# Performance work log

Measured on AMD Instinct MI355X. Metric: run time of the kernel, lower is better.

The kernel has to match this reference:

```python
import jax, jax.numpy as jnp
import numpy as np
from jax import lax

# Model dims (match init_kwargs)
D, K, V, H, R = 256, 16, 64, 4, 23
B, HH, WW = 16, 64, 64
EPS = 1e-5


def setup_inputs() -> dict:
    key = jax.random.key(0)
    ks = jax.random.split(key, 6)
    s = 0.05
    x = jax.random.normal(ks[0], (B, D, HH, WW), dtype=jnp.float32)
    Wq = jax.random.normal(ks[1], (H * K, D), dtype=jnp.float32) * s
    Wk = jax.random.normal(ks[2], (K, D), dtype=jnp.float32) * s
    Wv = jax.random.normal(ks[3], (V, D), dtype=jnp.float32) * s
    conv_w = jax.random.normal(ks[4], (K, 1, R, 1), dtype=jnp.float32) * s  # Conv2d(1, k, (r,1))
    conv_b = jnp.zeros((K,), jnp.float32)
    # BatchNorm (inference-mode) params for query and value branches
    q_gamma = jnp.ones((H * K,), jnp.float32)
    q_beta = jnp.zeros((H * K,), jnp.float32)
    q_mean = jnp.zeros((H * K,), jnp.float32)
    q_var = jnp.ones((H * K,), jnp.float32)
    v_gamma = jnp.ones((V,), jnp.float32)
    v_beta = jnp.zeros((V,), jnp.float32)
    v_mean = jnp.zeros((V,), jnp.float32)
    v_var = jnp.ones((V,), jnp.float32)
    return dict(x=x, Wq=Wq, q_gamma=q_gamma, q_beta=q_beta, q_mean=q_mean, q_var=q_var,
                Wk=Wk, Wv=Wv, v_gamma=v_gamma, v_beta=v_beta, v_mean=v_mean, v_var=v_var,
                conv_w=conv_w, conv_b=conv_b)


def _bn(y, g, b_, m, v_):
    # y: (b, c, n); per-channel affine normalization (eval-mode BatchNorm)
    scale = (g * lax.rsqrt(v_ + EPS))[None, :, None]
    return (y - m[None, :, None]) * scale + b_[None, :, None]


def reference(x, Wq, q_gamma, q_beta, q_mean, q_var, Wk, Wv, v_gamma, v_beta, v_mean, v_var, conv_w, conv_b):
    b, d, h, w = x.shape
    n = h * w
    xf = x.reshape(b, d, n)  # (b, d, n)

    # query: 1x1 conv -> BN -> (b, H, n, K)
    q = _bn(jnp.einsum('od,bdn->bon', Wq, xf), q_gamma, q_beta, q_mean, q_var)
    q = q.reshape(b, H, K, n).transpose(0, 1, 3, 2)  # (b, H, n, K)

    # key: 1x1 conv -> softmax over positions -> (b, n, K)
    kk = jax.nn.softmax(jnp.einsum('od,bdn->bon', Wk, xf), axis=-1).transpose(0, 2, 1)

    # value: 1x1 conv -> BN -> (b, n, V)
    vv = _bn(jnp.einsum('od,bdn->bon', Wv, xf), v_gamma, v_beta, v_mean, v_var).transpose(0, 2, 1)

    # content lambda: (b, K, V)
    lam_c = jnp.einsum('bmk,bmv->bkv', kk, vv)

    # position lambda via local conv over positions: (b, n, K, V)
    pad = (R - 1) // 2
    lam_p = lax.conv_general_dilated(
        vv[:, None, :, :], conv_w, window_strides=(1, 1),
        padding=[(pad, pad), (0, 0)],
        dimension_numbers=('NCHW', 'OIHW', 'NCHW'))  # (b, K, n, V)
    lam_p = lam_p + conv_b[None, :, None, None]
    lam_p = lam_p.transpose(0, 2, 1, 3)  # (b, n, K, V)

    # apply lambdas per position: (b, n, H, V)
    out = jnp.einsum('bhnk,bnkv->bnhv', q, lam_c[:, None, :, :] + lam_p)
    return out.reshape(b, h, w, H * V).transpose(0, 3, 1, 2)  # (b, H*V, h, w)
```

## Files before the change

### kernel.cpp

```cpp
#include <hip/hip_runtime.h>
#include <hip/hip_bf16.h>

typedef unsigned int uint;
typedef unsigned short ushort;

#define Bn 16
#define Dd 256
#define Nn 4096
#define Hh 4
#define Kk 16
#define Vv 64
#define Rr 23
#define Cc 144
#define NRT 9

typedef short bf16x8s __attribute__((ext_vector_type(8)));
typedef float f32x4 __attribute__((ext_vector_type(4)));
typedef float f32x8 __attribute__((ext_vector_type(8)));

static __device__ __forceinline__ ushort f2bf(float f) {
    __hip_bfloat16 h = __float2bfloat16(f);
    return __builtin_bit_cast(ushort, h);
}
static __device__ __forceinline__ float bf2f(ushort u) {
    return __uint_as_float(((uint)u) << 16);
}
static __device__ __forceinline__ float bflo(uint u) { return __uint_as_float(u << 16); }
static __device__ __forceinline__ float bfhi(uint u) { return __uint_as_float(u & 0xffff0000u); }

__global__ __launch_bounds__(256) void pack_kernel(
    const float* __restrict__ Wq, const float* __restrict__ qg, const float* __restrict__ qb,
    const float* __restrict__ qm, const float* __restrict__ qv,
    const float* __restrict__ Wk, const float* __restrict__ Wv,
    const float* __restrict__ vg, const float* __restrict__ vb,
    const float* __restrict__ vm, const float* __restrict__ vvar,
    const float* __restrict__ conv_w,
    ushort* __restrict__ Wf16, float* __restrict__ bias,
    ushort* __restrict__ cwf, float* __restrict__ num, float* __restrict__ den) {
    int c = blockIdx.x;
    int t = threadIdx.x;
    int d = t;
    float scale, bs;
    const float* src;
    if (c < 64) {
        scale = qg[c] * rsqrtf(qv[c] + 1e-5f);
        bs = qb[c] - qm[c] * scale;
        src = Wq + c * Dd;
    } else if (c < 80) {
        scale = 1.f; bs = 0.f;
        src = Wk + (c - 64) * Dd;
    } else {
        int j = c - 80;
        scale = vg[j] * rsqrtf(vvar[j] + 1e-5f);
        bs = vb[j] - vm[j] * scale;
        src = Wv + j * Dd;
    }
    int rt = c >> 4, lm = c & 15;
    int kk = d >> 5, hi = (d >> 3) & 3, j = d & 7;
    Wf16[((rt * 8 + kk) * 64 + hi * 16 + lm) * 8 + j] = f2bf(src[d] * scale);
    if (d == 0) bias[c] = bs;

    if (c == 0) {
#pragma unroll
        for (int m = 0; m < 4; m++) {
            int flat = t + 256 * m;
            int mt = flat >> 9, rem = flat & 511;
            int l = rem >> 3, jj = rem & 7;
            int r = mt * 16 + (l & 15);
            int k = (l >> 4) * 8 + jj;
            float v = (r < Rr && k < Kk) ? conv_w[k * Rr + r] : 0.f;
            cwf[flat] = f2bf(v);
        }
    }
    if (c == 1) {
        float4 z = {0.f, 0.f, 0.f, 0.f};
#pragma unroll
        for (int m = 0; m < 16; m++)
            reinterpret_cast<float4*>(num)[t + 256 * m] = z;
        if (t < 64) reinterpret_cast<float4*>(den)[t] = z;
    }
}

__global__ __launch_bounds__(256, 4) void proj_mfma_kernel(
    const float* __restrict__ x, const ushort* __restrict__ Wf16,
    const float* __restrict__ bias,
    ushort* __restrict__ qbufT, ushort* __restrict__ vbufT,
    float* __restrict__ num, float* __restrict__ den) {
    __shared__ ushort Wlds[NRT * 2 * 64 * 8];

    int b = blockIdx.y;
    int n0 = blockIdx.x * 64;
    int t = threadIdx.x;
    int w = t >> 6, l = t & 63;
    int lm = l & 15, hi = l >> 4;
    int n = n0 + w * 16 + lm;

    const uint* WfU = (const uint*)Wf16;
    uint* WldsU = (uint*)Wlds;

    f32x4 acc[NRT];
#pragma unroll
    for (int rt = 0; rt < NRT; rt++) acc[rt] = (f32x4){0.f, 0.f, 0.f, 0.f};

    const float* xb = x + (size_t)b * Dd * Nn + n;

    auto load8 = [&](int kk) -> f32x8 {
        const float* xp = xb + (size_t)(kk * 32 + hi * 8) * Nn;
        f32x8 r;
        r[0] = xp[0];
        r[1] = xp[(size_t)1 * Nn];
        r[2] = xp[(size_t)2 * Nn];
        r[3] = xp[(size_t)3 * Nn];
        r[4] = xp[(size_t)4 * Nn];
        r[5] = xp[(size_t)5 * Nn];
        r[6] = xp[(size_t)6 * Nn];
        r[7] = xp[(size_t)7 * Nn];
        return r;
    };
    auto cvt8 = [&](f32x8 f) -> bf16x8s {
        bf16x8s o;
#pragma unroll
        for (int j = 0; j < 8; j++) o[j] = (short)f2bf(f[j]);
        return o;
    };

    f32x8 xc0 = load8(0), xc1 = load8(1);
    f32x8 xn0 = xc0, xn1 = xc1;

#pragma unroll
    for (int p = 0; p < 4; p++) {
        int kb = p * 2;
        if (p) __syncthreads();
#pragma unroll
        for (int i = 0; i < 18; i++) {
            int flat = t + 256 * i;
            int f2 = flat >> 8;
            int rt = f2 >> 1, kkl = f2 & 1;
            WldsU[flat] = WfU[((rt * 8 + kb + kkl) << 8) + (flat & 255)];
        }
        __syncthreads();

        bf16x8s bf0 = cvt8(xc0);
        bf16x8s bf1 = cvt8(xc1);
        if (p < 3) {
            xn0 = load8(kb + 2);
            xn1 = load8(kb + 3);
        }
#pragma unroll
        for (int rt = 0; rt < NRT; rt++) {
            bf16x8s afrag = *reinterpret_cast<const bf16x8s*>(
                &Wlds[(size_t)((rt * 2 + 0) * 64 + l) * 8]);
            acc[rt] = __builtin_amdgcn_mfma_f32_16x16x32_bf16(afrag, bf0, acc[rt], 0, 0, 0);
        }
#pragma unroll
        for (int rt = 0; rt < NRT; rt++) {
            bf16x8s afrag = *reinterpret_cast<const bf16x8s*>(
                &Wlds[(size_t)((rt * 2 + 1) * 64 + l) * 8]);
            acc[rt] = __builtin_amdgcn_mfma_f32_16x16x32_bf16(afrag, bf1, acc[rt], 0, 0, 0);
        }
        xc0 = xn0;
        xc1 = xn1;
    }

    __syncthreads();
    {
        int nl = w * 16 + lm;
#pragma unroll
        for (int rt = 0; rt < 4; rt++)
#pragma unroll
            for (int rr = 0; rr < 4; rr++) {
                int kq = hi * 4 + rr;
                Wlds[nl * 72 + kq * 4 + rt] = f2bf(acc[rt][rr] + bias[rt * 16 + kq]);
            }
#pragma unroll
        for (int rt = 5; rt < 9; rt++)
#pragma unroll
            for (int rr = 0; rr < 4; rr++) {
                int v = (rt - 5) * 16 + hi * 4 + rr;
                Wlds[4608 + nl * 72 + v] = f2bf(acc[rt][rr] + bias[80 + v]);
            }
    }
    __syncthreads();

#pragma unroll
    for (int m = 0; m < 2; m++) {
        int i = t + 256 * m;
        int row = i >> 3, seg = i & 7;
        uint4 u = *reinterpret_cast<const uint4*>(&Wlds[row * 72 + seg * 8]);
        *reinterpret_cast<uint4*>(&qbufT[((size_t)b * Nn + n0 + row) * 64 + seg * 8]) = u;
    }
#pragma unroll
    for (int m = 0; m < 2; m++) {
        int i = t + 256 * m;
        int row = i >> 3, seg = i & 7;
        uint4 u = *reinterpret_cast<const uint4*>(&Wlds[4608 + row * 72 + seg * 8]);
        *reinterpret_cast<uint4*>(&vbufT[((size_t)b * Nn + n0 + row) * 64 + seg * 8]) = u;
    }

    float ev[4];
#pragma unroll
    for (int rr = 0; rr < 4; rr++)
        ev[rr] = __expf(acc[4][rr] + bias[64 + hi * 4 + rr]);
    __syncthreads();
    float* eks = reinterpret_cast<float*>(Wlds);
    {
        int nl = w * 16 + lm;
#pragma unroll
        for (int rr = 0; rr < 4; rr++)
            eks[(hi * 4 + rr) * 64 + nl] = ev[rr];
    }
    __syncthreads();
    {
        int v = t & 63, k0 = t >> 6;
        float a4[4] = {0.f, 0.f, 0.f, 0.f};
        for (int nl = 0; nl < 64; nl++) {
            float wv = bf2f(Wlds[4608 + nl * 72 + v]);
#pragma unroll
            for (int j2 = 0; j2 < 4; j2++)
                a4[j2] += eks[(k0 + 4 * j2) * 64 + nl] * wv;
        }
#pragma unroll
        for (int j2 = 0; j2 < 4; j2++)
            atomicAdd(&num[((size_t)b * Kk + k0 + 4 * j2) * Vv + v], a4[j2]);
        if (t < Kk) {
            float s = 0.f;
#pragma unroll
            for (int nl = 0; nl < 64; nl++) s += eks[t * 64 + nl];
            atomicAdd(&den[(size_t)b * Kk + t], s);
        }
    }
}

#define TN 32
__global__ __launch_bounds__(256, 4) void fused_out_kernel(
    const ushort* __restrict__ qbufT, const ushort* __restrict__ vbufT,
    const ushort* __restrict__ cwf, const float* __restrict__ num,
    const float* __restrict__ den, const float* __restrict__ conv_b,
    float* __restrict__ out) {
    __shared__ ushort Af[12 * 64 * 8];
    __shared__ ushort Sf[4][12 * 32 * 8];
    __shared__ ushort Qf[4][2 * 64 * 8];

    int b = blockIdx.y;
    int n0 = blockIdx.x * TN;
    int t = threadIdx.x;
    int l = t & 63;

    uint4 vld0 = {0, 0, 0, 0}, vld1 = {0, 0, 0, 0};
    {
        int c = t >> 3, vg = t & 7;
        int n = n0 - 11 + c;
        if (n >= 0 && n < Nn)
            vld0 = *reinterpret_cast<const uint4*>(&vbufT[((size_t)b * Nn + n) * 64 + vg * 8]);
        int i2 = t + 256;
        if (i2 < 432) {
            int c2 = i2 >> 3, vg2 = i2 & 7;
            int n2 = n0 - 11 + c2;
            if (n2 >= 0 && n2 < Nn)
                vld1 = *reinterpret_cast<const uint4*>(&vbufT[((size_t)b * Nn + n2) * 64 + vg2 * 8]);
        }
    }
    uint2 qld0, qld1;
    {
        int i = t;
        qld0 = *reinterpret_cast<const uint2*>(
            &qbufT[((size_t)b * Nn + n0 + (i & 31)) * 64 + (i >> 5) * 4]);
        int i2 = t + 256;
        qld1 = *reinterpret_cast<const uint2*>(
            &qbufT[((size_t)b * Nn + n0 + (i2 & 31)) * 64 + (i2 >> 5) * 4]);
    }
    uint4 cwld0 = *reinterpret_cast<const uint4*>(&cwf[(0 * 64 + l) * 8]);
    uint4 cwld1 = *reinterpret_cast<const uint4*>(&cwf[(1 * 64 + l) * 8]);
    float4 lcl = *reinterpret_cast<const float4*>(&num[(size_t)b * Kk * Vv + t * 4]);
    float dk = den[(size_t)b * Kk + (t >> 4)];
    float cb = conv_b[t >> 4];

    uint4 z4 = {0, 0, 0, 0};
    reinterpret_cast<uint4*>(Af)[512 + t] = z4;
#pragma unroll
    for (int m = 0; m < 6; m++) reinterpret_cast<uint4*>(Sf)[t + 256 * m] = z4;
#pragma unroll
    for (int m = 0; m < 2; m++) reinterpret_cast<uint4*>(Qf)[t + 256 * m] = z4;
    __syncthreads();

    {
        int c = t >> 3, vg = t & 7;
        int kk = c >> 5, hi = (c >> 3) & 3, j = c & 7;
        ushort* base = &Af[((kk * 4 + hi) * 64 + vg * 8) * 8 + j];
        uint va[4] = {vld0.x, vld0.y, vld0.z, vld0.w};
#pragma unroll
        for (int e = 0; e < 4; e++) {
            base[(2 * e + 0) * 8] = (ushort)(va[e] & 0xffff);
            base[(2 * e + 1) * 8] = (ushort)(va[e] >> 16);
        }
        int i2 = t + 256;
        if (i2 < 432) {
            int c2 = i2 >> 3, vg2 = i2 & 7;
            int kk2 = c2 >> 5, hi2 = (c2 >> 3) & 3, j2 = c2 & 7;
            ushort* base2 = &Af[((kk2 * 4 + hi2) * 64 + vg2 * 8) * 8 + j2];
            uint vb4[4] = {vld1.x, vld1.y, vld1.z, vld1.w};
#pragma unroll
            for (int e = 0; e < 4; e++) {
                base2[(2 * e + 0) * 8] = (ushort)(vb4[e] & 0xffff);
                base2[(2 * e + 1) * 8] = (ushort)(vb4[e] >> 16);
            }
        }
    }
    {
        int k = t >> 4, v0 = (t & 15) * 4;
        int c = 54 + k;
        int kk = c >> 5, hi = (c >> 3) & 3, j = c & 7;
        ushort* base = &Af[((kk * 4 + hi) * 64 + v0) * 8 + j];
        float inv = 1.f / dk;
        base[0]  = f2bf(lcl.x * inv + cb);
        base[8]  = f2bf(lcl.y * inv + cb);
        base[16] = f2bf(lcl.z * inv + cb);
        base[24] = f2bf(lcl.w * inv + cb);
    }
    {
        int i = t;
        {
            int k = i >> 5, nl = i & 31, m = 54 + k;
            int kk = m >> 5, hi = (m >> 3) & 3, j = m & 7;
            int off = ((kk * 4 + hi) * 32 + nl) * 8 + j;
            Sf[0][off] = (ushort)(qld0.x & 0xffff);
            Sf[1][off] = (ushort)(qld0.x >> 16);
            Sf[2][off] = (ushort)(qld0.y & 0xffff);
            Sf[3][off] = (ushort)(qld0.y >> 16);
            int nt = nl >> 4, lmq = nl & 15;
            int qoff = (nt * 64 + (k >> 3) * 16 + lmq) * 8 + (k & 7);
            Qf[0][qoff] = (ushort)(qld0.x & 0xffff);
            Qf[1][qoff] = (ushort)(qld0.x >> 16);
            Qf[2][qoff] = (ushort)(qld0.y & 0xffff);
            Qf[3][qoff] = (ushort)(qld0.y >> 16);
        }
        int i2 = t + 256;
        {
            int k = i2 >> 5, nl = i2 & 31, m = 54 + k;
            int kk = m >> 5, hi = (m >> 3) & 3, j = m & 7;
            int off = ((kk * 4 + hi) * 32 + nl) * 8 + j;
            Sf[0][off] = (ushort)(qld1.x & 0xffff);
            Sf[1][off] = (ushort)(qld1.x >> 16);
            Sf[2][off] = (ushort)(qld1.y & 0xffff);
            Sf[3][off] = (ushort)(qld1.y >> 16);
            int nt = nl >> 4, lmq = nl & 15;
            int qoff = (nt * 64 + (k >> 3) * 16 + lmq) * 8 + (k & 7);
            Qf[0][qoff] = (ushort)(qld1.x & 0xffff);
            Qf[1][qoff] = (ushort)(qld1.x >> 16);
            Qf[2][qoff] = (ushort)(qld1.y & 0xffff);
            Qf[3][qoff] = (ushort)(qld1.y >> 16);
        }
    }
    __syncthreads();

    int h = t >> 6;
    int lm = l & 15, hif = l >> 4;
    {
        bf16x8s cwfr0 = __builtin_bit_cast(bf16x8s, cwld0);
        bf16x8s cwfr1 = __builtin_bit_cast(bf16x8s, cwld1);
        f32x4 gacc[2][2];
#pragma unroll
        for (int nt = 0; nt < 2; nt++) {
            bf16x8s qfr = *reinterpret_cast<const bf16x8s*>(&Qf[h][(nt * 64 + l) * 8]);
            gacc[0][nt] = __builtin_amdgcn_mfma_f32_16x16x32_bf16(
                cwfr0, qfr, (f32x4){0.f, 0.f, 0.f, 0.f}, 0, 0, 0);
            gacc[1][nt] = __builtin_amdgcn_mfma_f32_16x16x32_bf16(
                cwfr1, qfr, (f32x4){0.f, 0.f, 0.f, 0.f}, 0, 0, 0);
        }
#pragma unroll
        for (int mt = 0; mt < 2; mt++)
#pragma unroll
            for (int nt = 0; nt < 2; nt++)
#pragma unroll
                for (int rr = 0; rr < 4; rr++) {
                    int r = mt * 16 + hif * 4 + rr;
                    if (r < Rr) {
                        int nl2 = nt * 16 + lm;
                        int m = nl2 + r;
                        Sf[h][((m >> 3) * 32 + nl2) * 8 + (m & 7)] = f2bf(gacc[mt][nt][rr]);
                    }
                }
    }
    __syncthreads();

    f32x4 acc[4][2];
#pragma unroll
    for (int mt = 0; mt < 4; mt++)
#pragma unroll
        for (int nt = 0; nt < 2; nt++) acc[mt][nt] = (f32x4){0.f, 0.f, 0.f, 0.f};

#pragma unroll
    for (int kk = 0; kk < 3; kk++) {
        bf16x8s bfr[2];
#pragma unroll
        for (int nt = 0; nt < 2; nt++)
            bfr[nt] = *reinterpret_cast<const bf16x8s*>(
                &Sf[h][((kk * 4 + hif) * 32 + nt * 16 + lm) * 8]);
#pragma unroll
        for (int mt = 0; mt < 4; mt++) {
            bf16x8s afr = *reinterpret_cast<const bf16x8s*>(
                &Af[((kk * 4 + hif) * 64 + mt * 16 + lm) * 8]);
#pragma unroll
            for (int nt = 0; nt < 2; nt++)
                acc[mt][nt] = __builtin_amdgcn_mfma_f32_16x16x32_bf16(afr, bfr[nt], acc[mt][nt], 0, 0, 0);
        }
    }

    float* ob = out + ((size_t)b * 256 + h * 64) * Nn + n0;
#pragma unroll
    for (int mt = 0; mt < 4; mt++)
#pragma unroll
        for (int nt = 0; nt < 2; nt++)
#pragma unroll
            for (int rr = 0; rr < 4; rr++) {
                int v = mt * 16 + hif * 4 + rr;
                ob[(size_t)v * Nn + nt * 16 + lm] = acc[mt][nt][rr];
            }
}

extern "C" void kernel_launch(void* const* d_in, const int* in_sizes, int n_in,
                              void* d_out, int out_size, void* d_ws, size_t ws_size,
                              hipStream_t stream) {
    const float* x      = (const float*)d_in[0];
    const float* Wq     = (const float*)d_in[1];
    const float* qg     = (const float*)d_in[2];
    const float* qb     = (const float*)d_in[3];
    const float* qm     = (const float*)d_in[4];
    const float* qv     = (const float*)d_in[5];
    const float* Wk     = (const float*)d_in[6];
    const float* Wv     = (const float*)d_in[7];
    const float* vg     = (const float*)d_in[8];
    const float* vb     = (const float*)d_in[9];
    const float* vm     = (const float*)d_in[10];
    const float* vvar   = (const float*)d_in[11];
    const float* conv_w = (const float*)d_in[12];
    const float* conv_b = (const float*)d_in[13];
    float* out = (float*)d_out;

    float* wsf = (float*)d_ws;
    ushort* Wf16  = (ushort*)wsf;
    float*  bias  = wsf + 18432;
    float*  num   = wsf + 18688;
    float*  den   = wsf + 35072;
    ushort* cwf   = (ushort*)(wsf + 35328);
    ushort* qbufT = (ushort*)(wsf + 35840);
    ushort* vbufT = (ushort*)(wsf + 2132992);

    pack_kernel<<<Cc, 256, 0, stream>>>(Wq, qg, qb, qm, qv, Wk, Wv, vg, vb, vm, vvar,
                                        conv_w, Wf16, bias, cwf, num, den);
    proj_mfma_kernel<<<dim3(Nn / 64, Bn), 256, 0, stream>>>(x, Wf16, bias,
                                                            qbufT, vbufT, num, den);
    fused_out_kernel<<<dim3(Nn / TN, Bn), 256, 0, stream>>>(qbufT, vbufT, cwf, num, den,
                                                            conv_b, out);
}
```

Measured before the change: 47.33 us.

## Shrink fused output kernel position tile from 32 to 16

Halves the number of positions each block of the fused output kernel handles. The shared-memory layout is rebuilt for the smaller tile: the halo window plus the lambda rows now fit in a reduction depth of 64 instead of 96, so two MFMA k-steps replace three. The aim is less wasted padding in the reduction and more blocks for latency hiding. The cost is twice as many blocks, a larger relative halo overhead on the value loads, and 16-wide output stores that coalesce less well.

```diff
diff --git a/kernel.cpp b/kernel.cpp
--- a/kernel.cpp
+++ b/kernel.cpp
@@ -231,15 +231,15 @@
     }
 }
 
-#define TN 32
+#define TN 16
 __global__ __launch_bounds__(256, 4) void fused_out_kernel(
     const ushort* __restrict__ qbufT, const ushort* __restrict__ vbufT,
     const ushort* __restrict__ cwf, const float* __restrict__ num,
     const float* __restrict__ den, const float* __restrict__ conv_b,
     float* __restrict__ out) {
-    __shared__ ushort Af[12 * 64 * 8];
-    __shared__ ushort Sf[4][12 * 32 * 8];
-    __shared__ ushort Qf[4][2 * 64 * 8];
+    __shared__ ushort Af[8 * 64 * 8];
+    __shared__ ushort Sf[4][8 * 16 * 8];
+    __shared__ ushort Qf[4][64 * 8];
 
     int b = blockIdx.y;
     int n0 = blockIdx.x * TN;
@@ -248,26 +248,23 @@
 
     uint4 vld0 = {0, 0, 0, 0}, vld1 = {0, 0, 0, 0};
     {
-        int c = t >> 3, vg = t & 7;
-        int n = n0 - 11 + c;
+        int j = t >> 3, seg = t & 7;
+        int n = n0 - 11 + j;
         if (n >= 0 && n < Nn)
-            vld0 = *reinterpret_cast<const uint4*>(&vbufT[((size_t)b * Nn + n) * 64 + vg * 8]);
+            vld0 = *reinterpret_cast<const uint4*>(&vbufT[((size_t)b * Nn + n) * 64 + seg * 8]);
         int i2 = t + 256;
-        if (i2 < 432) {
-            int c2 = i2 >> 3, vg2 = i2 & 7;
-            int n2 = n0 - 11 + c2;
+        if (i2 < 304) {
+            int j2 = i2 >> 3, seg2 = i2 & 7;
+            int n2 = n0 - 11 + j2;
             if (n2 >= 0 && n2 < Nn)
-                vld1 = *reinterpret_cast<const uint4*>(&vbufT[((size_t)b * Nn + n2) * 64 + vg2 * 8]);
-        }
-    }
-    uint2 qld0, qld1;
-    {
-        int i = t;
-        qld0 = *reinterpret_cast<const uint2*>(
-            &qbufT[((size_t)b * Nn + n0 + (i & 31)) * 64 + (i >> 5) * 4]);
-        int i2 = t + 256;
-        qld1 = *reinterpret_cast<const uint2*>(
-            &qbufT[((size_t)b * Nn + n0 + (i2 & 31)) * 64 + (i2 >> 5) * 4]);
+                vld1 = *reinterpret_cast<const uint4*>(&vbufT[((size_t)b * Nn + n2) * 64 + seg2 * 8]);
+        }
+    }
+    uint2 qld;
+    {
+        int nl = t >> 4, k = t & 15;
+        qld = *reinterpret_cast<const uint2*>(
+            &qbufT[((size_t)b * Nn + n0 + nl) * 64 + k * 4]);
     }
     uint4 cwld0 = *reinterpret_cast<const uint4*>(&cwf[(0 * 64 + l) * 8]);
     uint4 cwld1 = *reinterpret_cast<const uint4*>(&cwf[(1 * 64 + l) * 8]);
@@ -276,17 +273,16 @@
     float cb = conv_b[t >> 4];
 
     uint4 z4 = {0, 0, 0, 0};
-    reinterpret_cast<uint4*>(Af)[512 + t] = z4;
-#pragma unroll
-    for (int m = 0; m < 6; m++) reinterpret_cast<uint4*>(Sf)[t + 256 * m] = z4;
-#pragma unroll
-    for (int m = 0; m < 2; m++) reinterpret_cast<uint4*>(Qf)[t + 256 * m] = z4;
-    __syncthreads();
-
-    {
-        int c = t >> 3, vg = t & 7;
-        int kk = c >> 5, hi = (c >> 3) & 3, j = c & 7;
-        ushort* base = &Af[((kk * 4 + hi) * 64 + vg * 8) * 8 + j];
+    reinterpret_cast<uint4*>(Af)[t]       = z4;
+    reinterpret_cast<uint4*>(Af)[t + 256] = z4;
+    reinterpret_cast<uint4*>(Sf)[t]       = z4;
+    reinterpret_cast<uint4*>(Sf)[t + 256] = z4;
+    reinterpret_cast<uint4*>(Qf)[t]       = z4;
+    __syncthreads();
+
+    {
+        int c = t >> 3, seg = t & 7;
+        ushort* base = &Af[((c >> 3) * 64 + seg * 8) * 8 + (c & 7)];
         uint va[4] = {vld0.x, vld0.y, vld0.z, vld0.w};
 #pragma unroll
         for (int e = 0; e < 4; e++) {
@@ -294,10 +290,9 @@
             base[(2 * e + 1) * 8] = (ushort)(va[e] >> 16);
         }
         int i2 = t + 256;
-        if (i2 < 432) {
-            int c2 = i2 >> 3, vg2 = i2 & 7;
-            int kk2 = c2 >> 5, hi2 = (c2 >> 3) & 3, j2 = c2 & 7;
-            ushort* base2 = &Af[((kk2 * 4 + hi2) * 64 + vg2 * 8) * 8 + j2];
+        if (i2 < 304) {
+            int c2 = i2 >> 3, seg2 = i2 & 7;
+            ushort* base2 = &Af[((c2 >> 3) * 64 + seg2 * 8) * 8 + (c2 & 7)];
             uint vb4[4] = {vld1.x, vld1.y, vld1.z, vld1.w};
 #pragma unroll
             for (int e = 0; e < 4; e++) {
@@ -308,9 +303,8 @@
     }
     {
         int k = t >> 4, v0 = (t & 15) * 4;
-        int c = 54 + k;
-        int kk = c >> 5, hi = (c >> 3) & 3, j = c & 7;
-        ushort* base = &Af[((kk * 4 + hi) * 64 + v0) * 8 + j];
+        int c = 38 + k;
+        ushort* base = &Af[((c >> 3) * 64 + v0) * 8 + (c & 7)];
         float inv = 1.f / dk;
         base[0]  = f2bf(lcl.x * inv + cb);
         base[8]  = f2bf(lcl.y * inv + cb);
@@ -318,38 +312,18 @@
         base[24] = f2bf(lcl.w * inv + cb);
     }
     {
-        int i = t;
-        {
-            int k = i >> 5, nl = i & 31, m = 54 + k;
-            int kk = m >> 5, hi = (m >> 3) & 3, j = m & 7;
-            int off = ((kk * 4 + hi) * 32 + nl) * 8 + j;
-            Sf[0][off] = (ushort)(qld0.x & 0xffff);
-            Sf[1][off] = (ushort)(qld0.x >> 16);
-            Sf[2][off] = (ushort)(qld0.y & 0xffff);
-            Sf[3][off] = (ushort)(qld0.y >> 16);
-            int nt = nl >> 4, lmq = nl & 15;
-            int qoff = (nt * 64 + (k >> 3) * 16 + lmq) * 8 + (k & 7);
-            Qf[0][qoff] = (ushort)(qld0.x & 0xffff);
-            Qf[1][qoff] = (ushort)(qld0.x >> 16);
-            Qf[2][qoff] = (ushort)(qld0.y & 0xffff);
-            Qf[3][qoff] = (ushort)(qld0.y >> 16);
-        }
-        int i2 = t + 256;
-        {
-            int k = i2 >> 5, nl = i2 & 31, m = 54 + k;
-            int kk = m >> 5, hi = (m >> 3) & 3, j = m & 7;
-            int off = ((kk * 4 + hi) * 32 + nl) * 8 + j;
-            Sf[0][off] = (ushort)(qld1.x & 0xffff);
-            Sf[1][off] = (ushort)(qld1.x >> 16);
-            Sf[2][off] = (ushort)(qld1.y & 0xffff);
-            Sf[3][off] = (ushort)(qld1.y >> 16);
-            int nt = nl >> 4, lmq = nl & 15;
-            int qoff = (nt * 64 + (k >> 3) * 16 + lmq) * 8 + (k & 7);
-            Qf[0][qoff] = (ushort)(qld1.x & 0xffff);
-            Qf[1][qoff] = (ushort)(qld1.x >> 16);
-            Qf[2][qoff] = (ushort)(qld1.y & 0xffff);
-            Qf[3][qoff] = (ushort)(qld1.y >> 16);
-        }
+        int nl = t >> 4, k = t & 15;
+        int m = 38 + k;
+        int off = ((m >> 3) * 16 + nl) * 8 + (m & 7);
+        Sf[0][off] = (ushort)(qld.x & 0xffff);
+        Sf[1][off] = (ushort)(qld.x >> 16);
+        Sf[2][off] = (ushort)(qld.y & 0xffff);
+        Sf[3][off] = (ushort)(qld.y >> 16);
+        int qoff = ((k >> 3) * 16 + nl) * 8 + (k & 7);
+        Qf[0][qoff] = (ushort)(qld.x & 0xffff);
+        Qf[1][qoff] = (ushort)(qld.x >> 16);
+        Qf[2][qoff] = (ushort)(qld.y & 0xffff);
+        Qf[3][qoff] = (ushort)(qld.y >> 16);
     }
     __syncthreads();
 
@@ -358,51 +332,41 @@
     {
         bf16x8s cwfr0 = __builtin_bit_cast(bf16x8s, cwld0);
         bf16x8s cwfr1 = __builtin_bit_cast(bf16x8s, cwld1);
-        f32x4 gacc[2][2];
-#pragma unroll
-        for (int nt = 0; nt < 2; nt++) {
-            bf16x8s qfr = *reinterpret_cast<const bf16x8s*>(&Qf[h][(nt * 64 + l) * 8]);
-            gacc[0][nt] = __builtin_amdgcn_mfma_f32_16x16x32_bf16(
-                cwfr0, qfr, (f32x4){0.f, 0.f, 0.f, 0.f}, 0, 0, 0);
-            gacc[1][nt] = __builtin_amdgcn_mfma_f32_16x16x32_bf16(
-                cwfr1, qfr, (f32x4){0.f, 0.f, 0.f, 0.f}, 0, 0, 0);
-        }
-#pragma unroll
-        for (int mt = 0; mt < 2; mt++)
-#pragma unroll
-            for (int nt = 0; nt < 2; nt++)
-#pragma unroll
-                for (int rr = 0; rr < 4; rr++) {
-                    int r = mt * 16 + hif * 4 + rr;
-                    if (r < Rr) {
-                        int nl2 = nt * 16 + lm;
-                        int m = nl2 + r;
-                        Sf[h][((m >> 3) * 32 + nl2) * 8 + (m & 7)] = f2bf(gacc[mt][nt][rr]);
-                    }
-                }
-    }
-    __syncthreads();
-
-    f32x4 acc[4][2];
-#pragma unroll
-    for (int mt = 0; mt < 4; mt++)
-#pragma unroll
-        for (int nt = 0; nt < 2; nt++) acc[mt][nt] = (f32x4){0.f, 0.f, 0.f, 0.f};
-
-#pragma unroll
-    for (int kk = 0; kk < 3; kk++) {
-        bf16x8s bfr[2];
-#pragma unroll
-        for (int nt = 0; nt < 2; nt++)
-            bfr[nt] = *reinterpret_cast<const bf16x8s*>(
-                &Sf[h][((kk * 4 + hif) * 32 + nt * 16 + lm) * 8]);
+        bf16x8s qfr = *reinterpret_cast<const bf16x8s*>(&Qf[h][l * 8]);
+        f32x4 g0 = __builtin_amdgcn_mfma_f32_16x16x32_bf16(
+            cwfr0, qfr, (f32x4){0.f, 0.f, 0.f, 0.f}, 0, 0, 0);
+        f32x4 g1 = __builtin_amdgcn_mfma_f32_16x16x32_bf16(
+            cwfr1, qfr, (f32x4){0.f, 0.f, 0.f, 0.f}, 0, 0, 0);
+#pragma unroll
+        for (int rr = 0; rr < 4; rr++) {
+            int r = hif * 4 + rr;
+            int m = lm + r;
+            Sf[h][((m >> 3) * 16 + lm) * 8 + (m & 7)] = f2bf(g0[rr]);
+        }
+#pragma unroll
+        for (int rr = 0; rr < 4; rr++) {
+            int r = 16 + hif * 4 + rr;
+            if (r < Rr) {
+                int m = lm + r;
+                Sf[h][((m >> 3) * 16 + lm) * 8 + (m & 7)] = f2bf(g1[rr]);
+            }
+        }
+    }
+    __syncthreads();
+
+    f32x4 acc[4];
+#pragma unroll
+    for (int mt = 0; mt < 4; mt++) acc[mt] = (f32x4){0.f, 0.f, 0.f, 0.f};
+
+#pragma unroll
+    for (int kk = 0; kk < 2; kk++) {
+        bf16x8s bfr = *reinterpret_cast<const bf16x8s*>(
+            &Sf[h][((kk * 4 + hif) * 16 + lm) * 8]);
 #pragma unroll
         for (int mt = 0; mt < 4; mt++) {
             bf16x8s afr = *reinterpret_cast<const bf16x8s*>(
                 &Af[((kk * 4 + hif) * 64 + mt * 16 + lm) * 8]);
-#pragma unroll
-            for (int nt = 0; nt < 2; nt++)
-                acc[mt][nt] = __builtin_amdgcn_mfma_f32_16x16x32_bf16(afr, bfr[nt], acc[mt][nt], 0, 0, 0);
+            acc[mt] = __builtin_amdgcn_mfma_f32_16x16x32_bf16(afr, bfr, acc[mt], 0, 0, 0);
         }
     }
 
@@ -410,12 +374,10 @@
 #pragma unroll
     for (int mt = 0; mt < 4; mt++)
 #pragma unroll
-        for (int nt = 0; nt < 2; nt++)
-#pragma unroll
-            for (int rr = 0; rr < 4; rr++) {
-                int v = mt * 16 + hif * 4 + rr;
-                ob[(size_t)v * Nn + nt * 16 + lm] = acc[mt][nt][rr];
-            }
+        for (int rr = 0; rr < 4; rr++) {
+            int v = mt * 16 + hif * 4 + rr;
+            ob[(size_t)v * Nn + lm] = acc[mt][rr];
+        }
 }
 
 extern "C" void kernel_launch(void* const* d_in, const int* in_sizes, int n_in,
```

Result: slower. 50.60 us (+6.9%).
